# Kernel optimization log

Hardware: AMD Instinct MI355X
Metric: run time of the kernel (lower is better)

## Reference

```python
import jax, jax.numpy as jnp
import numpy as np

BH, L, D = 64, 1024, 128

def setup_inputs() -> dict:
    key = jax.random.key(0)
    k1, k2, k3 = jax.random.split(key, 3)
    q = jax.random.normal(k1, (BH, L, D), dtype=jnp.float32)
    k = jax.random.normal(k2, (BH, L, D), dtype=jnp.float32)
    v = jax.random.normal(k3, (BH, L, D), dtype=jnp.float32)
    # causal multiplicative mask, broadcast to all batch*head slices
    attn_mask = jnp.broadcast_to(jnp.tril(jnp.ones((L, L), dtype=jnp.float32)), (BH, L, L))
    return {"q": q, "k": k, "v": v, "attn_mask": attn_mask}

def reference(q, k, v, attn_mask):
    # NOTE: original module computes self.temper = dim_dec**0.5 but never uses it,
    # so scores are UNscaled. Dropout is identity at eval.
    attn = jnp.einsum('bqd,bkd->bqk', q, k)          # [BH, L, L]
    attn = attn * attn_mask                           # multiplicative mask on logits
    attn = jnp.exp(attn - jnp.max(attn))              # GLOBAL max subtraction (not per-row)
    attn = attn * attn_mask                           # mask again after exp
    attn = attn / (jnp.sum(attn, axis=2, keepdims=True) + 1e-15)
    return jnp.einsum('bqk,bkd->bqd', attn, v)        # [BH, L, D]
```

## Files before the change

### kernel.cpp

```cpp
#include <hip/hip_runtime.h>
#include <hip/hip_bf16.h>

#define BHN 64
#define LSEQ 1024
#define DIM 128
#define BM 128
#define BN 64
#define NQB (LSEQ / BM)

typedef _Float16 f16x4 __attribute__((ext_vector_type(4)));
typedef _Float16 f16x8 __attribute__((ext_vector_type(8)));
typedef float f32x4 __attribute__((ext_vector_type(4)));

__global__ __launch_bounds__(512, 4) void attn_pass1(
    const float* __restrict__ Q, const float* __restrict__ K,
    const float* __restrict__ V, float* __restrict__ Out,
    float* __restrict__ mrow, float* __restrict__ rrow, float* __restrict__ gmax)
{
    __shared__ _Float16 Kf[2][BN][132];
    __shared__ _Float16 Vt[2][DIM][68];

    const int tid  = threadIdx.x;
    const int wave = tid >> 6;
    const int lane = tid & 63;
    const int g    = lane >> 4;
    const int ln   = lane & 15;
    const int L    = blockIdx.x;
    const int i6   = (L >> 6) & 7;
    const int qb   = (L < 256) ? (NQB - 1 - i6) : (i6 & 3);
    const int bh   = L & 63;
    const int qrow0 = qb * BM + wave * 16;

    const float* qp = Q + (size_t)bh * LSEQ * DIM;
    const float* kp = K + (size_t)bh * LSEQ * DIM;
    const float* vp = V + (size_t)bh * LSEQ * DIM;

    const int vd = tid & 127;
    const int vh = tid >> 7;

    float4 kreg[4];
    float  vreg[2][8];

    auto issue = [&](int kv0) {
        #pragma unroll
        for (int i = 0; i < 4; ++i) {
            const int f4  = i * 512 + tid;
            const int row = f4 >> 5;
            const int c   = (f4 & 31) * 4;
            kreg[i] = *(const float4*)(kp + (size_t)(kv0 + row) * DIM + c);
        }
        #pragma unroll
        for (int nb = 0; nb < 2; ++nb)
            #pragma unroll
            for (int i = 0; i < 8; ++i)
                vreg[nb][i] = vp[(size_t)(kv0 + vh * 16 + nb * 8 + i) * DIM + vd];
    };

    auto convert_stage = [&](int b) {
        #pragma unroll
        for (int i = 0; i < 4; ++i) {
            const int f4  = i * 512 + tid;
            const int row = f4 >> 5;
            const int c   = (f4 & 31) * 4;
            f16x4 h4;
            h4[0] = (_Float16)kreg[i].x; h4[1] = (_Float16)kreg[i].y;
            h4[2] = (_Float16)kreg[i].z; h4[3] = (_Float16)kreg[i].w;
            *(f16x4*)&Kf[b][row][c] = h4;
        }
        #pragma unroll
        for (int nb = 0; nb < 2; ++nb) {
            f16x8 w;
            #pragma unroll
            for (int i = 0; i < 8; ++i) w[i] = (_Float16)vreg[nb][i];
            *(f16x8*)&Vt[b][vd][vh * 16 + nb * 8] = w;
        }
    };

    f16x8 qf[4];
    {
        const float* qrow = qp + (size_t)(qrow0 + ln) * DIM;
        #pragma unroll
        for (int kc = 0; kc < 4; ++kc) {
            const int d0 = kc * 32 + g * 8;
            float4 f0 = *(const float4*)(qrow + d0);
            float4 f1 = *(const float4*)(qrow + d0 + 4);
            f16x8 h;
            h[0] = (_Float16)f0.x; h[1] = (_Float16)f0.y;
            h[2] = (_Float16)f0.z; h[3] = (_Float16)f0.w;
            h[4] = (_Float16)f1.x; h[5] = (_Float16)f1.y;
            h[6] = (_Float16)f1.z; h[7] = (_Float16)f1.w;
            qf[kc] = h;
        }
    }

    float m_st = -1e30f, r_st = 0.f;
    f32x4 o_acc[8];
    #pragma unroll
    for (int d = 0; d < 8; ++d) { f32x4 z = {0.f,0.f,0.f,0.f}; o_acc[d] = z; }

    const int nt = 2 * qb + 2;

    issue(0);
    convert_stage(0);
    issue(BN);
    __syncthreads();

    int cur = 0;
    for (int t = 0; t < nt; ++t) {
        const int kv0 = t * BN;

        if (t + 1 < nt) {
            convert_stage(cur ^ 1);
            if (t + 2 < nt) issue((t + 2) * BN);
        }

        if (qrow0 + 15 >= kv0) {
            f32x4 sacc[4];
            #pragma unroll
            for (int ns = 0; ns < 4; ++ns) { f32x4 z = {0.f,0.f,0.f,0.f}; sacc[ns] = z; }
            __builtin_amdgcn_s_setprio(1);
            #pragma unroll
            for (int ns = 0; ns < 4; ++ns) {
                const int n = ns * 16 + ln;
                #pragma unroll
                for (int kc = 0; kc < 4; ++kc) {
                    f16x8 kh_ = *(const f16x8*)&Kf[cur][n][kc * 32 + g * 8];
                    sacc[ns] = __builtin_amdgcn_mfma_f32_16x16x32_f16(kh_, qf[kc], sacc[ns], 0, 0, 0);
                }
            }
            __builtin_amdgcn_s_setprio(0);

            if (kv0 + BN - 1 > qrow0) {
                const int qm = qrow0 + ln - kv0 - 4 * g;
                #pragma unroll
                for (int ns = 0; ns < 4; ++ns)
                    #pragma unroll
                    for (int j = 0; j < 4; ++j)
                        if (16 * ns + j > qm) sacc[ns][j] = -1e30f;
            }

            float tm = -1e30f;
            #pragma unroll
            for (int ns = 0; ns < 4; ++ns)
                #pragma unroll
                for (int j = 0; j < 4; ++j) tm = fmaxf(tm, sacc[ns][j]);
            tm = fmaxf(tm, __shfl_xor(tm, 16));
            tm = fmaxf(tm, __shfl_xor(tm, 32));
            const float mn = fmaxf(m_st, tm);
            const float sc = __expf(m_st - mn);
            float pr[4][4];
            float ts = 0.f;
            #pragma unroll
            for (int ns = 0; ns < 4; ++ns)
                #pragma unroll
                for (int j = 0; j < 4; ++j) {
                    const float pv = __expf(sacc[ns][j] - mn);
                    pr[ns][j] = pv;
                    ts += pv;
                }
            ts += __shfl_xor(ts, 16);
            ts += __shfl_xor(ts, 32);
            r_st = r_st * sc + ts;
            m_st = mn;

            float scr[4];
            #pragma unroll
            for (int r = 0; r < 4; ++r) scr[r] = __shfl(sc, 4 * g + r);
            #pragma unroll
            for (int d = 0; d < 8; ++d) {
                o_acc[d][0] *= scr[0]; o_acc[d][1] *= scr[1];
                o_acc[d][2] *= scr[2]; o_acc[d][3] *= scr[3];
            }

            f16x8 pa0, pa1;
            #pragma unroll
            for (int j = 0; j < 4; ++j) {
                pa0[j]     = (_Float16)pr[0][j];
                pa0[4 + j] = (_Float16)pr[1][j];
                pa1[j]     = (_Float16)pr[2][j];
                pa1[4 + j] = (_Float16)pr[3][j];
            }
            __builtin_amdgcn_s_setprio(1);
            #pragma unroll
            for (int ds = 0; ds < 8; ++ds) {
                const int dc = ds * 16 + ln;
                f16x4 v0 = *(const f16x4*)&Vt[cur][dc][4 * g];
                f16x4 v1 = *(const f16x4*)&Vt[cur][dc][16 + 4 * g];
                f16x8 bv0;
                #pragma unroll
                for (int j = 0; j < 4; ++j) { bv0[j] = v0[j]; bv0[4 + j] = v1[j]; }
                o_acc[ds] = __builtin_amdgcn_mfma_f32_16x16x32_f16(pa0, bv0, o_acc[ds], 0, 0, 0);
                f16x4 v2 = *(const f16x4*)&Vt[cur][dc][32 + 4 * g];
                f16x4 v3 = *(const f16x4*)&Vt[cur][dc][48 + 4 * g];
                f16x8 bv1;
                #pragma unroll
                for (int j = 0; j < 4; ++j) { bv1[j] = v2[j]; bv1[4 + j] = v3[j]; }
                o_acc[ds] = __builtin_amdgcn_mfma_f32_16x16x32_f16(pa1, bv1, o_acc[ds], 0, 0, 0);
            }
            __builtin_amdgcn_s_setprio(0);
        }

        __syncthreads();
        cur ^= 1;
    }

    #pragma unroll
    for (int ds = 0; ds < 8; ++ds) {
        const int dc = ds * 16 + ln;
        #pragma unroll
        for (int r = 0; r < 4; ++r) {
            const int qr = qrow0 + g * 4 + r;
            Out[((size_t)bh * LSEQ + qr) * DIM + dc] = o_acc[ds][r];
        }
    }
    if (lane < 16) {
        mrow[bh * LSEQ + qrow0 + lane] = m_st;
        rrow[bh * LSEQ + qrow0 + lane] = r_st;
    }
    float bm = m_st;
    #pragma unroll
    for (int off = 32; off >= 1; off >>= 1) bm = fmaxf(bm, __shfl_xor(bm, off));
    if (lane == 0) atomicMax((int*)gmax, __float_as_int(bm));
}

__global__ __launch_bounds__(256) void attn_epilogue(
    float* __restrict__ Out, const float* __restrict__ mrow,
    const float* __restrict__ rrow, const float* __restrict__ gmax)
{
    const int idx = blockIdx.x * 256 + threadIdx.x;
    const int row = idx >> 5;
    const float M = *gmax;
    float e = M - mrow[row] - 34.538776394910684f;
    e = fminf(e, 85.f);
    const float denom = rrow[row] + __expf(e);
    const float inv = 1.0f / denom;
    float4 o = ((float4*)Out)[idx];
    o.x *= inv; o.y *= inv; o.z *= inv; o.w *= inv;
    ((float4*)Out)[idx] = o;
}

extern "C" void kernel_launch(void* const* d_in, const int* in_sizes, int n_in,
                              void* d_out, int out_size, void* d_ws, size_t ws_size,
                              hipStream_t stream)
{
    const float* q = (const float*)d_in[0];
    const float* k = (const float*)d_in[1];
    const float* v = (const float*)d_in[2];
    float* out  = (float*)d_out;
    float* mrow = (float*)d_ws;
    float* rrow = mrow + BHN * LSEQ;
    float* gmax = rrow + BHN * LSEQ;

    hipMemsetAsync(gmax, 0, sizeof(float), stream);

    attn_pass1<<<dim3(BHN * NQB), 512, 0, stream>>>(q, k, v, out, mrow, rrow, gmax);

    const int n4 = BHN * LSEQ * DIM / 4;
    attn_epilogue<<<n4 / 256, 256, 0, stream>>>(out, mrow, rrow, gmax);
}
```

Measured before the change: 91.27 us.

## Split KV range of each query block across two workgroups and merge in epilogue

Each query block's causal KV range is now split into two halves, each handled by its own workgroup, which doubles the grid and balances per-block work. Partial outputs, row maxes and row sums go to separate buffers, and the epilogue merges them with rescaled weights before normalising. This is meant to cut load imbalance and tail effects from causal blocks of very different lengths. The cost is an extra full-size partial output buffer, plus more epilogue reads and writes.

```diff
diff --git a/kernel.cpp b/kernel.cpp
--- a/kernel.cpp
+++ b/kernel.cpp
@@ -7,6 +7,7 @@
 #define BM 128
 #define BN 64
 #define NQB (LSEQ / BM)
+#define NROW (BHN * LSEQ)
 
 typedef _Float16 f16x4 __attribute__((ext_vector_type(4)));
 typedef _Float16 f16x8 __attribute__((ext_vector_type(8)));
@@ -15,7 +16,7 @@
 __global__ __launch_bounds__(512, 4) void attn_pass1(
     const float* __restrict__ Q, const float* __restrict__ K,
     const float* __restrict__ V, float* __restrict__ Out,
-    float* __restrict__ mrow, float* __restrict__ rrow, float* __restrict__ gmax)
+    float* __restrict__ PO1, float* __restrict__ mr, float* __restrict__ gmax)
 {
     __shared__ _Float16 Kf[2][BN][132];
     __shared__ _Float16 Vt[2][DIM][68];
@@ -26,14 +27,19 @@
     const int g    = lane >> 4;
     const int ln   = lane & 15;
     const int L    = blockIdx.x;
-    const int i6   = (L >> 6) & 7;
-    const int qb   = (L < 256) ? (NQB - 1 - i6) : (i6 & 3);
+    const int qb   = (NQB - 1) - (L >> 7);
+    const int c    = (L >> 6) & 1;
     const int bh   = L & 63;
+    const int base = c * (qb + 1);
+    const int nt   = qb + 1;
     const int qrow0 = qb * BM + wave * 16;
 
     const float* qp = Q + (size_t)bh * LSEQ * DIM;
     const float* kp = K + (size_t)bh * LSEQ * DIM;
     const float* vp = V + (size_t)bh * LSEQ * DIM;
+    float* po    = c ? PO1 : Out;
+    float* mbase = mr + c * (2 * NROW);
+    float* rbase = mbase + NROW;
 
     const int vd = tid & 127;
     const int vh = tid >> 7;
@@ -46,8 +52,8 @@
         for (int i = 0; i < 4; ++i) {
             const int f4  = i * 512 + tid;
             const int row = f4 >> 5;
-            const int c   = (f4 & 31) * 4;
-            kreg[i] = *(const float4*)(kp + (size_t)(kv0 + row) * DIM + c);
+            const int cc  = (f4 & 31) * 4;
+            kreg[i] = *(const float4*)(kp + (size_t)(kv0 + row) * DIM + cc);
         }
         #pragma unroll
         for (int nb = 0; nb < 2; ++nb)
@@ -61,11 +67,11 @@
         for (int i = 0; i < 4; ++i) {
             const int f4  = i * 512 + tid;
             const int row = f4 >> 5;
-            const int c   = (f4 & 31) * 4;
+            const int cc  = (f4 & 31) * 4;
             f16x4 h4;
             h4[0] = (_Float16)kreg[i].x; h4[1] = (_Float16)kreg[i].y;
             h4[2] = (_Float16)kreg[i].z; h4[3] = (_Float16)kreg[i].w;
-            *(f16x4*)&Kf[b][row][c] = h4;
+            *(f16x4*)&Kf[b][row][cc] = h4;
         }
         #pragma unroll
         for (int nb = 0; nb < 2; ++nb) {
@@ -98,20 +104,18 @@
     #pragma unroll
     for (int d = 0; d < 8; ++d) { f32x4 z = {0.f,0.f,0.f,0.f}; o_acc[d] = z; }
 
-    const int nt = 2 * qb + 2;
-
-    issue(0);
+    issue(base * BN);
     convert_stage(0);
-    issue(BN);
+    issue((base + 1) * BN);
     __syncthreads();
 
     int cur = 0;
     for (int t = 0; t < nt; ++t) {
-        const int kv0 = t * BN;
+        const int kv0 = (base + t) * BN;
 
         if (t + 1 < nt) {
             convert_stage(cur ^ 1);
-            if (t + 2 < nt) issue((t + 2) * BN);
+            if (t + 2 < nt) issue((base + t + 2) * BN);
         }
 
         if (qrow0 + 15 >= kv0) {
@@ -210,12 +214,12 @@
         #pragma unroll
         for (int r = 0; r < 4; ++r) {
             const int qr = qrow0 + g * 4 + r;
-            Out[((size_t)bh * LSEQ + qr) * DIM + dc] = o_acc[ds][r];
+            po[((size_t)bh * LSEQ + qr) * DIM + dc] = o_acc[ds][r];
         }
     }
     if (lane < 16) {
-        mrow[bh * LSEQ + qrow0 + lane] = m_st;
-        rrow[bh * LSEQ + qrow0 + lane] = r_st;
+        mbase[bh * LSEQ + qrow0 + lane] = m_st;
+        rbase[bh * LSEQ + qrow0 + lane] = r_st;
     }
     float bm = m_st;
     #pragma unroll
@@ -224,18 +228,27 @@
 }
 
 __global__ __launch_bounds__(256) void attn_epilogue(
-    float* __restrict__ Out, const float* __restrict__ mrow,
-    const float* __restrict__ rrow, const float* __restrict__ gmax)
+    float* __restrict__ Out, const float* __restrict__ PO1,
+    const float* __restrict__ mr, const float* __restrict__ gmax)
 {
     const int idx = blockIdx.x * 256 + threadIdx.x;
     const int row = idx >> 5;
-    const float M = *gmax;
-    float e = M - mrow[row] - 34.538776394910684f;
-    e = fminf(e, 85.f);
-    const float denom = rrow[row] + __expf(e);
-    const float inv = 1.0f / denom;
-    float4 o = ((float4*)Out)[idx];
-    o.x *= inv; o.y *= inv; o.z *= inv; o.w *= inv;
+    const float M  = *gmax;
+    const float m0 = mr[row],            r0 = mr[NROW + row];
+    const float m1 = mr[2 * NROW + row], r1 = mr[3 * NROW + row];
+    const float m  = fmaxf(m0, m1);
+    const float e0 = __expf(m0 - m);
+    const float e1 = __expf(m1 - m);
+    const float ee = __expf(fminf(M - m - 34.538776394910684f, 85.f));
+    const float inv = 1.0f / (r0 * e0 + r1 * e1 + ee);
+    const float w0 = e0 * inv, w1 = e1 * inv;
+    float4 a = ((const float4*)Out)[idx];
+    float4 b = ((const float4*)PO1)[idx];
+    float4 o;
+    o.x = a.x * w0 + b.x * w1;
+    o.y = a.y * w0 + b.y * w1;
+    o.z = a.z * w0 + b.z * w1;
+    o.w = a.w * w0 + b.w * w1;
     ((float4*)Out)[idx] = o;
 }
 
@@ -247,14 +260,14 @@
     const float* k = (const float*)d_in[1];
     const float* v = (const float*)d_in[2];
     float* out  = (float*)d_out;
-    float* mrow = (float*)d_ws;
-    float* rrow = mrow + BHN * LSEQ;
-    float* gmax = rrow + BHN * LSEQ;
+    float* po1  = (float*)d_ws;
+    float* mr   = po1 + (size_t)NROW * DIM;
+    float* gmax = mr + 4 * NROW;
 
     hipMemsetAsync(gmax, 0, sizeof(float), stream);
 
-    attn_pass1<<<dim3(BHN * NQB), 512, 0, stream>>>(q, k, v, out, mrow, rrow, gmax);
-
-    const int n4 = BHN * LSEQ * DIM / 4;
-    attn_epilogue<<<n4 / 256, 256, 0, stream>>>(out, mrow, rrow, gmax);
+    attn_pass1<<<dim3(2 * NQB * BHN), 512, 0, stream>>>(q, k, v, out, po1, mr, gmax);
+
+    const int n4 = NROW * DIM / 4;
+    attn_epilogue<<<n4 / 256, 256, 0, stream>>>(out, po1, mr, gmax);
 }
```

Result: slower. 148.1 us (+62.3%).
